# Performance work log

Hardware: AMD Instinct MI355X
Metric: run time of the kernel (lower is better)

Reference implementation:

```python
import jax, jax.numpy as jnp
import numpy as np

B, T = 512, 200          # batch (trials), time bins
N = 10000                # n_neurons
SI, DI = 100, 68         # static / dynamic input sizes
HS, HD = 256, 128        # hidden_dim_static / hidden_dim_dynamic
K = 1                    # output_size
D = 2 * HD + HS          # 512, routed-GEMM contraction dim


def setup_inputs() -> dict:
    key = jax.random.key(0)
    ks = jax.random.split(key, 19)
    g = lambda i, shape, s=0.05: (jax.random.normal(ks[i], shape, jnp.float32) * s)
    return dict(
        x_static=g(0, (B, SI), 1.0),
        x_dynamic=g(1, (B, T, DI), 1.0),
        neuron_order=jax.random.randint(ks[2], (B,), 0, N),
        w_s1=g(3, (HS, SI)), b_s1=g(4, (HS,)),
        w_s2=g(5, (HS, HS)), b_s2=g(6, (HS,)),
        w_dyn=g(7, (HD, DI)), b_dyn=g(8, (HD,)),
        w_ih_f=g(9, (HD, HD)), w_hh_f=g(10, (HD, HD)),
        b_ih_f=g(11, (HD,)), b_hh_f=g(12, (HD,)),
        w_ih_b=g(13, (HD, HD)), w_hh_b=g(14, (HD, HD)),
        b_ih_b=g(15, (HD,)), b_hh_b=g(16, (HD,)),
        neuron_weights=g(17, (N, D, K)),
        neuron_bias=g(18, (N, 1, K)),
    )


def _rnn_dir(x, w_ih, w_hh, b_ih, b_hh, reverse):
    # x: [B,T,H] -> outputs [B,T,H]; torch nn.RNN with nonlinearity='relu'
    xw = jnp.einsum('bth,oh->bto', x, w_ih) + b_ih + b_hh  # precompute input proj
    h0 = jnp.zeros((x.shape[0], w_hh.shape[0]), x.dtype)

    def step(h, xt):
        h = jax.nn.relu(xt + h @ w_hh.T)
        return h, h

    _, ys = jax.lax.scan(step, h0, jnp.swapaxes(xw, 0, 1), reverse=reverse)
    return jnp.swapaxes(ys, 0, 1)


def reference(x_static, x_dynamic, neuron_order,
              w_s1, b_s1, w_s2, b_s2, w_dyn, b_dyn,
              w_ih_f, w_hh_f, b_ih_f, b_hh_f,
              w_ih_b, w_hh_b, b_ih_b, b_hh_b,
              neuron_weights, neuron_bias):
    # static branch (dropout in eval mode -> identity)
    s = jax.nn.relu(x_static @ w_s1.T + b_s1)
    s = jax.nn.relu(s @ w_s2.T + b_s2)                      # [B,HS]
    # dynamic branch
    d = jax.nn.relu(jnp.einsum('bti,oi->bto', x_dynamic, w_dyn) + b_dyn)  # [B,T,HD]
    fwd = _rnn_dir(d, w_ih_f, w_hh_f, b_ih_f, b_hh_f, reverse=False)
    bwd = _rnn_dir(d, w_ih_b, w_hh_b, b_ih_b, b_hh_b, reverse=True)
    d = jax.nn.relu(jnp.concatenate([fwd, bwd], axis=-1))   # [B,T,2*HD]
    # tile static over time and concat
    s_t = jnp.broadcast_to(s[:, None, :], (s.shape[0], d.shape[1], s.shape[1]))
    final_input = jnp.concatenate([s_t, d], axis=-1)        # [B,T,D]
    # per-sample neuron weight gather + routed batched matmul + bias + ReLU
    Wn = neuron_weights[neuron_order]                       # [B,D,K]
    bn = neuron_bias[neuron_order]                          # [B,1,K]
    out = jnp.einsum('btd,bdk->btk', final_input, Wn) + bn  # [B,T,K]
    return jax.nn.relu(jnp.squeeze(out, -1))                # [B,T] (K=1)
```

## Files before the change

### kernel.cpp

```cpp
#include <hip/hip_runtime.h>
#include <cstdint>

constexpr int B = 512, T = 200, SI = 100, DI = 68, HS = 256, HD = 128, D = 512;
constexpr int BT = B * T;

typedef __attribute__((ext_vector_type(8))) short short8;
typedef __attribute__((ext_vector_type(4))) float floatx4;
typedef _Float16 half8 __attribute__((ext_vector_type(8)));
typedef _Float16 half2t __attribute__((ext_vector_type(2)));
typedef unsigned int uint2v __attribute__((ext_vector_type(2)));
typedef unsigned int uint4v __attribute__((ext_vector_type(4)));

#define DEV __device__ __forceinline__

DEV unsigned short f2bf(float f) {
    unsigned int x = __builtin_bit_cast(unsigned int, f);
    x += 0x7fffu + ((x >> 16) & 1u);
    return (unsigned short)(x >> 16);
}
DEV unsigned int pkbf(float a, float b) {
    return (unsigned int)f2bf(a) | ((unsigned int)f2bf(b) << 16);
}
DEV unsigned short f2h(float f) {
    return __builtin_bit_cast(unsigned short, (_Float16)f);
}
DEV half2t u2h2(unsigned int u) { return __builtin_bit_cast(half2t, u); }
DEV unsigned int pkh(float a, float b) {
    return __builtin_bit_cast(unsigned int, __builtin_amdgcn_cvt_pkrtz(a, b));
}
#if __has_builtin(__builtin_amdgcn_permlane32_swap) && __has_builtin(__builtin_amdgcn_permlane16_swap)
DEV void pl32swap(unsigned int& a, unsigned int& b) {
    uint2v r = __builtin_amdgcn_permlane32_swap(a, b, false, false);
    a = r[0]; b = r[1];
}
DEV void pl16swap(unsigned int& a, unsigned int& b) {
    uint2v r = __builtin_amdgcn_permlane16_swap(a, b, false, false);
    a = r[0]; b = r[1];
}
#else
DEV void pl32swap(unsigned int& a, unsigned int& b) {
    unsigned int na, nb;
    asm("v_mov_b32 %0, %2\n\t"
        "v_mov_b32 %1, %3\n\t"
        "v_permlane32_swap_b32 %0, %1"
        : "=&v"(na), "=&v"(nb) : "v"(a), "v"(b));
    a = na; b = nb;
}
DEV void pl16swap(unsigned int& a, unsigned int& b) {
    unsigned int na, nb;
    asm("v_mov_b32 %0, %2\n\t"
        "v_mov_b32 %1, %3\n\t"
        "v_permlane16_swap_b32 %0, %1"
        : "=&v"(na), "=&v"(nb) : "v"(a), "v"(b));
    a = na; b = nb;
}
#endif

__global__ __launch_bounds__(256) void k_prep(
    const float* __restrict__ wdyn,
    const float* __restrict__ wihf, const float* __restrict__ wihb,
    const float* __restrict__ whhf, const float* __restrict__ whhb,
    const float* __restrict__ bihf, const float* __restrict__ bhhf,
    const float* __restrict__ bihb, const float* __restrict__ bhhb,
    unsigned short* __restrict__ wdyn_bf, unsigned short* __restrict__ wih_bf,
    unsigned short* __restrict__ whh_h, float* __restrict__ bsum)
{
    int gid = blockIdx.x * 256 + threadIdx.x, gs = gridDim.x * 256;
    for (int i = gid; i < HD * 96; i += gs) {
        int r = i / 96, c = i - r * 96;
        wdyn_bf[i] = (c < DI) ? f2bf(wdyn[r * DI + c]) : 0;
    }
    for (int i = gid; i < 2 * HD * HD; i += gs) {
        const float* src = (i < HD * HD) ? wihf : wihb;
        wih_bf[i] = f2bf(src[i & (HD * HD - 1)]);
    }
    for (int i = gid; i < 2 * HD * HD; i += gs) {
        const float* src = (i < HD * HD) ? whhf : whhb;
        whh_h[i] = f2h(src[i & (HD * HD - 1)]);
    }
    for (int i = gid; i < 2 * HD; i += gs) {
        int z = i >> 7, n = i & (HD - 1);
        bsum[i] = z ? (bihb[n] + bhhb[n]) : (bihf[n] + bhhf[n]);
    }
}

__global__ __launch_bounds__(256) void k_static(
    const float* __restrict__ xs_g, const float* __restrict__ w1,
    const float* __restrict__ b1, const float* __restrict__ w2,
    const float* __restrict__ b2, const int* __restrict__ norder,
    const float* __restrict__ nw, const float* __restrict__ nb,
    float* __restrict__ statd)
{
    __shared__ __align__(16) float xs[SI];
    __shared__ __align__(16) float s1[HS];
    __shared__ __align__(16) float red[256];
    int b = blockIdx.x, t = threadIdx.x;
    if (t < SI) xs[t] = xs_g[b * SI + t];
    __syncthreads();
    float a = b1[t];
    const float4* w = (const float4*)(w1 + t * SI);
    const float4* xp4 = (const float4*)xs;
    #pragma unroll
    for (int i = 0; i < SI / 4; ++i) {
        float4 ww = w[i]; float4 xx = xp4[i];
        a += xx.x * ww.x + xx.y * ww.y + xx.z * ww.z + xx.w * ww.w;
    }
    s1[t] = fmaxf(a, 0.f);
    __syncthreads();
    float a2 = b2[t];
    const float4* w2p = (const float4*)(w2 + t * HS);
    const float4* s1p = (const float4*)s1;
    #pragma unroll 8
    for (int i = 0; i < HS / 4; ++i) {
        float4 ww = w2p[i]; float4 s = s1p[i];
        a2 += s.x * ww.x + s.y * ww.y + s.z * ww.z + s.w * ww.w;
    }
    float sv = fmaxf(a2, 0.f);
    int n = norder[b];
    red[t] = sv * nw[(size_t)n * D + t];
    __syncthreads();
    for (int s = 128; s > 0; s >>= 1) {
        if (t < s) red[t] += red[t + s];
        __syncthreads();
    }
    if (t == 0) statd[b] = red[0] + nb[n];
}

__global__ __launch_bounds__(256) void k_dxw(
    const float* __restrict__ xd,
    const unsigned short* __restrict__ wdyn_bf, const float* __restrict__ bdyn,
    const unsigned short* __restrict__ wih_bf, const float* __restrict__ bsum,
    unsigned short* __restrict__ xw)
{
    __shared__ __align__(16) unsigned short xb[64][104];
    __shared__ __align__(16) unsigned short dl[64][136];
    int tid = threadIdx.x;
    int R0 = blockIdx.x * 64;
    for (int i = tid; i < 64 * 104 / 8; i += 256)
        ((uint4v*)xb)[i] = uint4v{0u, 0u, 0u, 0u};
    __syncthreads();
    for (int i = tid; i < 64 * 17; i += 256) {
        int r = i / 17, c = i - r * 17;
        float4 v = *(const float4*)(xd + (size_t)(R0 + r) * DI + c * 4);
        uint2 pk;
        pk.x = pkbf(v.x, v.y);
        pk.y = pkbf(v.z, v.w);
        *(uint2*)&xb[r][c * 4] = pk;
    }
    __syncthreads();

    int lane = tid & 63, w = tid >> 6;
    int ln = lane & 15, q = lane >> 4;

    short8 xf[3];
    #pragma unroll
    for (int c = 0; c < 3; ++c)
        xf[c] = *(const short8*)&xb[w * 16 + ln][c * 32 + q * 8];
    #pragma unroll
    for (int j = 0; j < 8; ++j) {
        floatx4 a = {0.f, 0.f, 0.f, 0.f};
        #pragma unroll
        for (int c = 0; c < 3; ++c) {
            short8 wf = *(const short8*)(wdyn_bf + (size_t)(j * 16 + ln) * 96 + c * 32 + q * 8);
            a = __builtin_amdgcn_mfma_f32_16x16x32_bf16(wf, xf[c], a, 0, 0, 0);
        }
        float4 bd4 = *(const float4*)(bdyn + j * 16 + q * 4);
        uint2 pk;
        pk.x = pkbf(fmaxf(a[0] + bd4.x, 0.f), fmaxf(a[1] + bd4.y, 0.f));
        pk.y = pkbf(fmaxf(a[2] + bd4.z, 0.f), fmaxf(a[3] + bd4.w, 0.f));
        *(uint2*)&dl[w * 16 + ln][j * 16 + q * 4] = pk;
    }
    __syncthreads();

    short8 df[4];
    #pragma unroll
    for (int c = 0; c < 4; ++c)
        df[c] = *(const short8*)&dl[w * 16 + ln][c * 32 + q * 8];
    #pragma unroll
    for (int z = 0; z < 2; ++z) {
        const unsigned short* wih = wih_bf + (size_t)z * HD * HD;
        unsigned short* outp = xw + (size_t)z * BT * HD;
        int row = R0 + w * 16 + ln;
        #pragma unroll
        for (int j = 0; j < 8; ++j) {
            floatx4 a = {0.f, 0.f, 0.f, 0.f};
            #pragma unroll
            for (int c = 0; c < 4; ++c) {
                short8 wf = *(const short8*)(wih + (size_t)(j * 16 + ln) * HD + c * 32 + q * 8);
                a = __builtin_amdgcn_mfma_f32_16x16x32_bf16(wf, df[c], a, 0, 0, 0);
            }
            float4 b4 = *(const float4*)(bsum + z * HD + j * 16 + q * 4);
            uint2 hp;
            hp.x = (unsigned int)f2h(a[0] + b4.x) | ((unsigned int)f2h(a[1] + b4.y) << 16);
            hp.y = (unsigned int)f2h(a[2] + b4.z) | ((unsigned int)f2h(a[3] + b4.w) << 16);
            *(uint2*)(outp + (size_t)row * HD + j * 16 + q * 4) = hp;
        }
    }
}

__global__ __launch_bounds__(256, 1) void k_scan(
    const unsigned short* __restrict__ xw, const unsigned short* __restrict__ whh_h,
    const int* __restrict__ norder, const float* __restrict__ nw,
    float* __restrict__ accf, float* __restrict__ accb)
{
    __shared__ __align__(16) uint4v hxch[2][4][64];
    __shared__ __align__(16) float  pxch[2][4][16];

    int tid = threadIdx.x, w = tid >> 6, l = tid & 63, ln = l & 15, q = l >> 4;
    int dir = blockIdx.x >> 5, b0 = (blockIdx.x & 31) * 16;
    const unsigned short* whh = whh_h + (size_t)dir * HD * HD;
    float* acc = dir ? accb : accf;
    int segoff = dir ? (HS + HD) : HS;
    int j0 = 2 * w;

    half8 wfr[2][4];
    #pragma unroll
    for (int jj = 0; jj < 2; ++jj)
        #pragma unroll
        for (int c = 0; c < 4; ++c)
            wfr[jj][c] = *(const half8*)(whh + (size_t)((j0 + jj) * 16 + ln) * HD + c * 32 + q * 8);

    int nrow = norder[b0 + ln];
    float4 wnl[2];
    #pragma unroll
    for (int jj = 0; jj < 2; ++jj)
        wnl[jj] = *(const float4*)(nw + (size_t)nrow * D + segoff + (j0 + jj) * 16 + q * 4);

    half8 hf[4];
    uint4v zz = {0u, 0u, 0u, 0u};
    #pragma unroll
    for (int c = 0; c < 4; ++c) hf[c] = __builtin_bit_cast(half8, zz);

    const unsigned short* xp = xw + ((size_t)dir * BT + (size_t)(b0 + ln) * T) * HD;
    float* accp = acc + (size_t)(b0 + ln) * T;
    int tstart = dir ? (T - 1) : 0, dt = dir ? -1 : 1;

    uint2 xb0[2], xb1[2], xb2[2], xb3[2];
    auto ld = [&](uint2 (&xb)[2], int idx) {
        const unsigned short* pp = xp + (size_t)(tstart + dt * idx) * HD;
        #pragma unroll
        for (int jj = 0; jj < 2; ++jj)
            xb[jj] = *(const uint2*)(pp + (j0 + jj) * 16 + q * 4);
    };
    auto step = [&](uint2 (&xc)[2], int idx) {
        int t = tstart + dt * idx;
        int par = idx & 1;
        floatx4 a[2];
        #pragma unroll
        for (int jj = 0; jj < 2; ++jj) {
            half2t lo = u2h2(xc[jj].x), hi = u2h2(xc[jj].y);
            a[jj] = floatx4{(float)lo[0], (float)lo[1], (float)hi[0], (float)hi[1]};
        }
        #pragma unroll
        for (int cc = 0; cc < 4; ++cc)
            #pragma unroll
            for (int jj = 0; jj < 2; ++jj)
                a[jj] = __builtin_amdgcn_mfma_f32_16x16x32_f16(wfr[jj][cc], hf[cc], a[jj], 0, 0, 0);
        uint2 hp[2];
        float p = 0.f;
        #pragma unroll
        for (int jj = 0; jj < 2; ++jj) {
            float r0 = fmaxf(a[jj][0], 0.f), r1 = fmaxf(a[jj][1], 0.f);
            float r2 = fmaxf(a[jj][2], 0.f), r3 = fmaxf(a[jj][3], 0.f);
            hp[jj].x = pkh(r0, r1);
            hp[jj].y = pkh(r2, r3);
            float4 wn4 = wnl[jj];
            p += r0 * wn4.x + r1 * wn4.y + r2 * wn4.z + r3 * wn4.w;
        }
        unsigned int ax = hp[0].x, bx = hp[1].x;
        pl32swap(ax, bx); pl16swap(ax, bx);
        unsigned int ay = hp[0].y, by = hp[1].y;
        pl32swap(ay, by); pl16swap(ay, by);
        uint4v hw = {ax, ay, bx, by};
        hxch[par][w][l] = hw;
        unsigned int pa = __builtin_bit_cast(unsigned int, p), pb = pa;
        pl32swap(pa, pb);
        float ps = __builtin_bit_cast(float, pa) + __builtin_bit_cast(float, pb);
        unsigned int pc = __builtin_bit_cast(unsigned int, ps), pd = pc;
        pl16swap(pc, pd);
        float ptot = __builtin_bit_cast(float, pc) + __builtin_bit_cast(float, pd);
        if (l < 16) pxch[par][w][ln] = ptot;
        asm volatile("s_waitcnt lgkmcnt(0)" ::: "memory");
        __builtin_amdgcn_sched_barrier(0);
        __builtin_amdgcn_s_barrier();
        __builtin_amdgcn_sched_barrier(0);
        #pragma unroll
        for (int c = 0; c < 4; ++c)
            hf[c] = __builtin_bit_cast(half8, hxch[par][c][l]);
        if (w == 0) {
            float p2 = pxch[par][q][ln];
            unsigned int qa = __builtin_bit_cast(unsigned int, p2), qb = qa;
            pl32swap(qa, qb);
            float qs = __builtin_bit_cast(float, qa) + __builtin_bit_cast(float, qb);
            unsigned int qc = __builtin_bit_cast(unsigned int, qs), qd = qc;
            pl16swap(qc, qd);
            float qt = __builtin_bit_cast(float, qc) + __builtin_bit_cast(float, qd);
            if (l < 16) accp[t] = qt;
        }
    };

    ld(xb0, 0); ld(xb1, 1); ld(xb2, 2); ld(xb3, 3);
    for (int c = 0; c < T / 4 - 1; ++c) {
        int i0 = c * 4;
        step(xb0, i0);     ld(xb0, i0 + 4);
        step(xb1, i0 + 1); ld(xb1, i0 + 5);
        step(xb2, i0 + 2); ld(xb2, i0 + 6);
        step(xb3, i0 + 3); ld(xb3, i0 + 7);
    }
    step(xb0, T - 4);
    step(xb1, T - 3);
    step(xb2, T - 2);
    step(xb3, T - 1);
}

__global__ __launch_bounds__(256) void k_final(
    const float* __restrict__ statd, const float* __restrict__ accf,
    const float* __restrict__ accb, float* __restrict__ out)
{
    int idx = blockIdx.x * 256 + threadIdx.x;
    if (idx < BT) {
        int b = idx / T;
        out[idx] = fmaxf(statd[b] + accf[idx] + accb[idx], 0.f);
    }
}

extern "C" void kernel_launch(void* const* d_in, const int* in_sizes, int n_in,
                              void* d_out, int out_size, void* d_ws, size_t ws_size,
                              hipStream_t stream)
{
    const float* x_static  = (const float*)d_in[0];
    const float* x_dynamic = (const float*)d_in[1];
    const int*   norder    = (const int*)d_in[2];
    const float* w_s1   = (const float*)d_in[3];
    const float* b_s1   = (const float*)d_in[4];
    const float* w_s2   = (const float*)d_in[5];
    const float* b_s2   = (const float*)d_in[6];
    const float* w_dyn  = (const float*)d_in[7];
    const float* b_dyn  = (const float*)d_in[8];
    const float* w_ih_f = (const float*)d_in[9];
    const float* w_hh_f = (const float*)d_in[10];
    const float* b_ih_f = (const float*)d_in[11];
    const float* b_hh_f = (const float*)d_in[12];
    const float* w_ih_b = (const float*)d_in[13];
    const float* w_hh_b = (const float*)d_in[14];
    const float* b_ih_b = (const float*)d_in[15];
    const float* b_hh_b = (const float*)d_in[16];
    const float* nw     = (const float*)d_in[17];
    const float* nb     = (const float*)d_in[18];
    float* out = (float*)d_out;

    char* ws = (char*)d_ws;
    float* statd = (float*)ws;
    float* accf  = (float*)(ws + 2048);
    float* accb  = (float*)(ws + 2048 + (size_t)BT * 4);
    unsigned short* xw = (unsigned short*)(ws + 2048 + (size_t)BT * 8);
    size_t xw_bytes = (size_t)2 * BT * HD * 2;
    unsigned short* wdyn_bf = (unsigned short*)(ws + 2048 + (size_t)BT * 8 + xw_bytes);
    unsigned short* wih_bf  = wdyn_bf + HD * 96;
    unsigned short* whh_h   = wih_bf + 2 * HD * HD;
    float* bsum = (float*)(whh_h + 2 * HD * HD);

    hipLaunchKernelGGL(k_prep, dim3(64), dim3(256), 0, stream,
                       w_dyn, w_ih_f, w_ih_b, w_hh_f, w_hh_b,
                       b_ih_f, b_hh_f, b_ih_b, b_hh_b,
                       wdyn_bf, wih_bf, whh_h, bsum);
    hipLaunchKernelGGL(k_static, dim3(B), dim3(256), 0, stream,
                       x_static, w_s1, b_s1, w_s2, b_s2, norder, nw, nb, statd);
    hipLaunchKernelGGL(k_dxw, dim3(BT / 64), dim3(256), 0, stream,
                       x_dynamic, wdyn_bf, b_dyn, wih_bf, bsum, xw);
    hipLaunchKernelGGL(k_scan, dim3(64), dim3(256), 0, stream,
                       xw, whh_h, norder, nw, accf, accb);
    hipLaunchKernelGGL(k_final, dim3((BT + 255) / 256), dim3(256), 0, stream,
                       statd, accf, accb, out);
}
```

Measured before the change: 299.2 us.

## Interleave forward and backward RNN scans in one block, drop partial-sum LDS exchange

```diff
diff --git a/kernel.cpp b/kernel.cpp
--- a/kernel.cpp
+++ b/kernel.cpp
@@ -203,114 +203,143 @@
     const int* __restrict__ norder, const float* __restrict__ nw,
     float* __restrict__ accf, float* __restrict__ accb)
 {
-    __shared__ __align__(16) uint4v hxch[2][4][64];
-    __shared__ __align__(16) float  pxch[2][4][16];
+    __shared__ __align__(16) uint4v hxch[2][2][4][64];
 
     int tid = threadIdx.x, w = tid >> 6, l = tid & 63, ln = l & 15, q = l >> 4;
-    int dir = blockIdx.x >> 5, b0 = (blockIdx.x & 31) * 16;
-    const unsigned short* whh = whh_h + (size_t)dir * HD * HD;
-    float* acc = dir ? accb : accf;
-    int segoff = dir ? (HS + HD) : HS;
+    int b0 = blockIdx.x * 16;
     int j0 = 2 * w;
 
-    half8 wfr[2][4];
-    #pragma unroll
-    for (int jj = 0; jj < 2; ++jj)
-        #pragma unroll
-        for (int c = 0; c < 4; ++c)
-            wfr[jj][c] = *(const half8*)(whh + (size_t)((j0 + jj) * 16 + ln) * HD + c * 32 + q * 8);
+    half8 wfr[2][2][4];
+    #pragma unroll
+    for (int d = 0; d < 2; ++d)
+        #pragma unroll
+        for (int jj = 0; jj < 2; ++jj)
+            #pragma unroll
+            for (int c = 0; c < 4; ++c)
+                wfr[d][jj][c] = *(const half8*)(whh_h + (size_t)d * HD * HD +
+                    (size_t)((j0 + jj) * 16 + ln) * HD + c * 32 + q * 8);
 
     int nrow = norder[b0 + ln];
-    float4 wnl[2];
-    #pragma unroll
-    for (int jj = 0; jj < 2; ++jj)
-        wnl[jj] = *(const float4*)(nw + (size_t)nrow * D + segoff + (j0 + jj) * 16 + q * 4);
-
-    half8 hf[4];
+    float4 wnl[2][2];
+    #pragma unroll
+    for (int d = 0; d < 2; ++d)
+        #pragma unroll
+        for (int jj = 0; jj < 2; ++jj)
+            wnl[d][jj] = *(const float4*)(nw + (size_t)nrow * D + (d ? HS + HD : HS) +
+                                          (j0 + jj) * 16 + q * 4);
+
+    half8 hfF[4], hfB[4];
     uint4v zz = {0u, 0u, 0u, 0u};
     #pragma unroll
-    for (int c = 0; c < 4; ++c) hf[c] = __builtin_bit_cast(half8, zz);
-
-    const unsigned short* xp = xw + ((size_t)dir * BT + (size_t)(b0 + ln) * T) * HD;
-    float* accp = acc + (size_t)(b0 + ln) * T;
-    int tstart = dir ? (T - 1) : 0, dt = dir ? -1 : 1;
-
-    uint2 xb0[2], xb1[2], xb2[2], xb3[2];
-    auto ld = [&](uint2 (&xb)[2], int idx) {
-        const unsigned short* pp = xp + (size_t)(tstart + dt * idx) * HD;
-        #pragma unroll
-        for (int jj = 0; jj < 2; ++jj)
-            xb[jj] = *(const uint2*)(pp + (j0 + jj) * 16 + q * 4);
+    for (int c = 0; c < 4; ++c) {
+        hfF[c] = __builtin_bit_cast(half8, zz);
+        hfB[c] = __builtin_bit_cast(half8, zz);
+    }
+
+    const unsigned short* xpF = xw + ((size_t)(b0 + ln) * T) * HD;
+    const unsigned short* xpB = xw + ((size_t)BT + (size_t)(b0 + ln) * T) * HD;
+    float* accpF = accf + (size_t)w * BT + (size_t)(b0 + ln) * T;
+    float* accpB = accb + (size_t)w * BT + (size_t)(b0 + ln) * T;
+
+    uint2 xF0[2], xF1[2], xF2[2], xF3[2];
+    uint2 xB0[2], xB1[2], xB2[2], xB3[2];
+    auto ld = [&](uint2 (&xF)[2], uint2 (&xB)[2], int idx) {
+        const unsigned short* ppF = xpF + (size_t)idx * HD;
+        const unsigned short* ppB = xpB + (size_t)(T - 1 - idx) * HD;
+        #pragma unroll
+        for (int jj = 0; jj < 2; ++jj) {
+            xF[jj] = *(const uint2*)(ppF + (j0 + jj) * 16 + q * 4);
+            xB[jj] = *(const uint2*)(ppB + (j0 + jj) * 16 + q * 4);
+        }
     };
-    auto step = [&](uint2 (&xc)[2], int idx) {
-        int t = tstart + dt * idx;
+    auto step = [&](uint2 (&xF)[2], uint2 (&xB)[2], int idx) {
+        int tF = idx, tB = T - 1 - idx;
         int par = idx & 1;
-        floatx4 a[2];
+        floatx4 aF[2], aB[2];
         #pragma unroll
         for (int jj = 0; jj < 2; ++jj) {
-            half2t lo = u2h2(xc[jj].x), hi = u2h2(xc[jj].y);
-            a[jj] = floatx4{(float)lo[0], (float)lo[1], (float)hi[0], (float)hi[1]};
-        }
-        #pragma unroll
-        for (int cc = 0; cc < 4; ++cc)
+            half2t lo = u2h2(xF[jj].x), hi = u2h2(xF[jj].y);
+            aF[jj] = floatx4{(float)lo[0], (float)lo[1], (float)hi[0], (float)hi[1]};
+            half2t lo2 = u2h2(xB[jj].x), hi2 = u2h2(xB[jj].y);
+            aB[jj] = floatx4{(float)lo2[0], (float)lo2[1], (float)hi2[0], (float)hi2[1]};
+        }
+        #pragma unroll
+        for (int cc = 0; cc < 4; ++cc) {
             #pragma unroll
             for (int jj = 0; jj < 2; ++jj)
-                a[jj] = __builtin_amdgcn_mfma_f32_16x16x32_f16(wfr[jj][cc], hf[cc], a[jj], 0, 0, 0);
-        uint2 hp[2];
-        float p = 0.f;
+                aF[jj] = __builtin_amdgcn_mfma_f32_16x16x32_f16(wfr[0][jj][cc], hfF[cc], aF[jj], 0, 0, 0);
+            #pragma unroll
+            for (int jj = 0; jj < 2; ++jj)
+                aB[jj] = __builtin_amdgcn_mfma_f32_16x16x32_f16(wfr[1][jj][cc], hfB[cc], aB[jj], 0, 0, 0);
+        }
+        uint2 hpF[2], hpB[2];
+        float pF = 0.f, pB = 0.f;
         #pragma unroll
         for (int jj = 0; jj < 2; ++jj) {
-            float r0 = fmaxf(a[jj][0], 0.f), r1 = fmaxf(a[jj][1], 0.f);
-            float r2 = fmaxf(a[jj][2], 0.f), r3 = fmaxf(a[jj][3], 0.f);
-            hp[jj].x = pkh(r0, r1);
-            hp[jj].y = pkh(r2, r3);
-            float4 wn4 = wnl[jj];
-            p += r0 * wn4.x + r1 * wn4.y + r2 * wn4.z + r3 * wn4.w;
-        }
-        unsigned int ax = hp[0].x, bx = hp[1].x;
-        pl32swap(ax, bx); pl16swap(ax, bx);
-        unsigned int ay = hp[0].y, by = hp[1].y;
-        pl32swap(ay, by); pl16swap(ay, by);
-        uint4v hw = {ax, ay, bx, by};
-        hxch[par][w][l] = hw;
-        unsigned int pa = __builtin_bit_cast(unsigned int, p), pb = pa;
+            float r0 = fmaxf(aF[jj][0], 0.f), r1 = fmaxf(aF[jj][1], 0.f);
+            float r2 = fmaxf(aF[jj][2], 0.f), r3 = fmaxf(aF[jj][3], 0.f);
+            hpF[jj].x = pkh(r0, r1); hpF[jj].y = pkh(r2, r3);
+            float4 wn4 = wnl[0][jj];
+            pF += r0 * wn4.x + r1 * wn4.y + r2 * wn4.z + r3 * wn4.w;
+            float s0 = fmaxf(aB[jj][0], 0.f), s1 = fmaxf(aB[jj][1], 0.f);
+            float s2 = fmaxf(aB[jj][2], 0.f), s3 = fmaxf(aB[jj][3], 0.f);
+            hpB[jj].x = pkh(s0, s1); hpB[jj].y = pkh(s2, s3);
+            float4 wm4 = wnl[1][jj];
+            pB += s0 * wm4.x + s1 * wm4.y + s2 * wm4.z + s3 * wm4.w;
+        }
+        {
+            unsigned int ax = hpF[0].x, bx = hpF[1].x;
+            pl32swap(ax, bx); pl16swap(ax, bx);
+            unsigned int ay = hpF[0].y, by = hpF[1].y;
+            pl32swap(ay, by); pl16swap(ay, by);
+            hxch[par][0][w][l] = uint4v{ax, ay, bx, by};
+        }
+        {
+            unsigned int ax = hpB[0].x, bx = hpB[1].x;
+            pl32swap(ax, bx); pl16swap(ax, bx);
+            unsigned int ay = hpB[0].y, by = hpB[1].y;
+            pl32swap(ay, by); pl16swap(ay, by);
+            hxch[par][1][w][l] = uint4v{ax, ay, bx, by};
+        }
+        unsigned int pa = __builtin_bit_cast(unsigned int, pF), pb = pa;
         pl32swap(pa, pb);
         float ps = __builtin_bit_cast(float, pa) + __builtin_bit_cast(float, pb);
         unsigned int pc = __builtin_bit_cast(unsigned int, ps), pd = pc;
         pl16swap(pc, pd);
-        float ptot = __builtin_bit_cast(float, pc) + __builtin_bit_cast(float, pd);
-        if (l < 16) pxch[par][w][ln] = ptot;
+        float ptF = __builtin_bit_cast(float, pc) + __builtin_bit_cast(float, pd);
+        unsigned int qa = __builtin_bit_cast(unsigned int, pB), qb = qa;
+        pl32swap(qa, qb);
+        float qs = __builtin_bit_cast(float, qa) + __builtin_bit_cast(float, qb);
+        unsigned int qc = __builtin_bit_cast(unsigned int, qs), qd = qc;
+        pl16swap(qc, qd);
+        float ptB = __builtin_bit_cast(float, qc) + __builtin_bit_cast(float, qd);
+        if (l < 16) {
+            accpF[tF] = ptF;
+            accpB[tB] = ptB;
+        }
         asm volatile("s_waitcnt lgkmcnt(0)" ::: "memory");
         __builtin_amdgcn_sched_barrier(0);
         __builtin_amdgcn_s_barrier();
         __builtin_amdgcn_sched_barrier(0);
         #pragma unroll
-        for (int c = 0; c < 4; ++c)
-            hf[c] = __builtin_bit_cast(half8, hxch[par][c][l]);
-        if (w == 0) {
-            float p2 = pxch[par][q][ln];
-            unsigned int qa = __builtin_bit_cast(unsigned int, p2), qb = qa;
-            pl32swap(qa, qb);
-            float qs = __builtin_bit_cast(float, qa) + __builtin_bit_cast(float, qb);
-            unsigned int qc = __builtin_bit_cast(unsigned int, qs), qd = qc;
-            pl16swap(qc, qd);
-            float qt = __builtin_bit_cast(float, qc) + __builtin_bit_cast(float, qd);
-            if (l < 16) accp[t] = qt;
+        for (int c = 0; c < 4; ++c) {
+            hfF[c] = __builtin_bit_cast(half8, hxch[par][0][c][l]);
+            hfB[c] = __builtin_bit_cast(half8, hxch[par][1][c][l]);
         }
     };
 
-    ld(xb0, 0); ld(xb1, 1); ld(xb2, 2); ld(xb3, 3);
+    ld(xF0, xB0, 0); ld(xF1, xB1, 1); ld(xF2, xB2, 2); ld(xF3, xB3, 3);
     for (int c = 0; c < T / 4 - 1; ++c) {
         int i0 = c * 4;
-        step(xb0, i0);     ld(xb0, i0 + 4);
-        step(xb1, i0 + 1); ld(xb1, i0 + 5);
-        step(xb2, i0 + 2); ld(xb2, i0 + 6);
-        step(xb3, i0 + 3); ld(xb3, i0 + 7);
-    }
-    step(xb0, T - 4);
-    step(xb1, T - 3);
-    step(xb2, T - 2);
-    step(xb3, T - 1);
+        step(xF0, xB0, i0);     ld(xF0, xB0, i0 + 4);
+        step(xF1, xB1, i0 + 1); ld(xF1, xB1, i0 + 5);
+        step(xF2, xB2, i0 + 2); ld(xF2, xB2, i0 + 6);
+        step(xF3, xB3, i0 + 3); ld(xF3, xB3, i0 + 7);
+    }
+    step(xF0, xB0, T - 4);
+    step(xF1, xB1, T - 3);
+    step(xF2, xB2, T - 2);
+    step(xF3, xB3, T - 1);
 }
 
 __global__ __launch_bounds__(256) void k_final(
@@ -320,7 +349,11 @@
     int idx = blockIdx.x * 256 + threadIdx.x;
     if (idx < BT) {
         int b = idx / T;
-        out[idx] = fmaxf(statd[b] + accf[idx] + accb[idx], 0.f);
+        float s = statd[b];
+        #pragma unroll
+        for (int w = 0; w < 4; ++w)
+            s += accf[(size_t)w * BT + idx] + accb[(size_t)w * BT + idx];
+        out[idx] = fmaxf(s, 0.f);
     }
 }
 
@@ -352,10 +385,10 @@
     char* ws = (char*)d_ws;
     float* statd = (float*)ws;
     float* accf  = (float*)(ws + 2048);
-    float* accb  = (float*)(ws + 2048 + (size_t)BT * 4);
-    unsigned short* xw = (unsigned short*)(ws + 2048 + (size_t)BT * 8);
+    float* accb  = (float*)(ws + 2048 + (size_t)4 * BT * 4);
+    unsigned short* xw = (unsigned short*)(ws + 2048 + (size_t)8 * BT * 4);
     size_t xw_bytes = (size_t)2 * BT * HD * 2;
-    unsigned short* wdyn_bf = (unsigned short*)(ws + 2048 + (size_t)BT * 8 + xw_bytes);
+    unsigned short* wdyn_bf = (unsigned short*)(ws + 2048 + (size_t)8 * BT * 4 + xw_bytes);
     unsigned short* wih_bf  = wdyn_bf + HD * 96;
     unsigned short* whh_h   = wih_bf + 2 * HD * HD;
     float* bsum = (float*)(whh_h + 2 * HD * HD);
@@ -368,7 +401,7 @@
                        x_static, w_s1, b_s1, w_s2, b_s2, norder, nw, nb, statd);
     hipLaunchKernelGGL(k_dxw, dim3(BT / 64), dim3(256), 0, stream,
                        x_dynamic, wdyn_bf, b_dyn, wih_bf, bsum, xw);
-    hipLaunchKernelGGL(k_scan, dim3(64), dim3(256), 0, stream,
+    hipLaunchKernelGGL(k_scan, dim3(32), dim3(256), 0, stream,
                        xw, whh_h, norder, nw, accf, accb);
     hipLaunchKernelGGL(k_final, dim3((BT + 255) / 256), dim3(256), 0, stream,
                        statd, accf, accb, out);
```

Result: slower. 348.5 us (+16.5%).

## Split RNN scan across 8 waves per block and defer projection reduction

Applied to the files above, without the earlier changes.

```diff
diff --git a/kernel.cpp b/kernel.cpp
--- a/kernel.cpp
+++ b/kernel.cpp
@@ -198,88 +198,70 @@
     }
 }
 
-__global__ __launch_bounds__(256, 1) void k_scan(
+__global__ __launch_bounds__(512, 1) void k_scan(
     const unsigned short* __restrict__ xw, const unsigned short* __restrict__ whh_h,
     const int* __restrict__ norder, const float* __restrict__ nw,
     float* __restrict__ accf, float* __restrict__ accb)
 {
     __shared__ __align__(16) uint4v hxch[2][4][64];
-    __shared__ __align__(16) float  pxch[2][4][16];
 
     int tid = threadIdx.x, w = tid >> 6, l = tid & 63, ln = l & 15, q = l >> 4;
     int dir = blockIdx.x >> 5, b0 = (blockIdx.x & 31) * 16;
     const unsigned short* whh = whh_h + (size_t)dir * HD * HD;
-    float* acc = dir ? accb : accf;
+    float* acc = (dir ? accb : accf) + (size_t)w * BT;
     int segoff = dir ? (HS + HD) : HS;
-    int j0 = 2 * w;
-
-    half8 wfr[2][4];
-    #pragma unroll
-    for (int jj = 0; jj < 2; ++jj)
-        #pragma unroll
-        for (int c = 0; c < 4; ++c)
-            wfr[jj][c] = *(const half8*)(whh + (size_t)((j0 + jj) * 16 + ln) * HD + c * 32 + q * 8);
+
+    half8 wfr[4];
+    #pragma unroll
+    for (int c = 0; c < 4; ++c)
+        wfr[c] = *(const half8*)(whh + (size_t)(w * 16 + ln) * HD + c * 32 + q * 8);
 
     int nrow = norder[b0 + ln];
-    float4 wnl[2];
-    #pragma unroll
-    for (int jj = 0; jj < 2; ++jj)
-        wnl[jj] = *(const float4*)(nw + (size_t)nrow * D + segoff + (j0 + jj) * 16 + q * 4);
+    float4 wnl = *(const float4*)(nw + (size_t)nrow * D + segoff + w * 16 + q * 4);
 
     half8 hf[4];
     uint4v zz = {0u, 0u, 0u, 0u};
     #pragma unroll
     for (int c = 0; c < 4; ++c) hf[c] = __builtin_bit_cast(half8, zz);
 
-    const unsigned short* xp = xw + ((size_t)dir * BT + (size_t)(b0 + ln) * T) * HD;
+    const unsigned short* xp = xw + ((size_t)dir * BT + (size_t)(b0 + ln) * T) * HD
+                               + w * 16 + q * 4;
     float* accp = acc + (size_t)(b0 + ln) * T;
     int tstart = dir ? (T - 1) : 0, dt = dir ? -1 : 1;
 
-    uint2 xb0[2], xb1[2], xb2[2], xb3[2];
-    auto ld = [&](uint2 (&xb)[2], int idx) {
-        const unsigned short* pp = xp + (size_t)(tstart + dt * idx) * HD;
-        #pragma unroll
-        for (int jj = 0; jj < 2; ++jj)
-            xb[jj] = *(const uint2*)(pp + (j0 + jj) * 16 + q * 4);
+    int wc = w >> 1;
+    int qp = 2 * (w & 1) + (q >> 1);
+    int boff = (q & 1) * 8;
+
+    uint2 x0, x1, x2, x3;
+    auto ld = [&](uint2& xb, int idx) {
+        xb = *(const uint2*)(xp + (size_t)(tstart + dt * idx) * HD);
     };
-    auto step = [&](uint2 (&xc)[2], int idx) {
+    auto step = [&](uint2& xc, int idx) {
         int t = tstart + dt * idx;
         int par = idx & 1;
-        floatx4 a[2];
-        #pragma unroll
-        for (int jj = 0; jj < 2; ++jj) {
-            half2t lo = u2h2(xc[jj].x), hi = u2h2(xc[jj].y);
-            a[jj] = floatx4{(float)lo[0], (float)lo[1], (float)hi[0], (float)hi[1]};
-        }
-        #pragma unroll
-        for (int cc = 0; cc < 4; ++cc)
-            #pragma unroll
-            for (int jj = 0; jj < 2; ++jj)
-                a[jj] = __builtin_amdgcn_mfma_f32_16x16x32_f16(wfr[jj][cc], hf[cc], a[jj], 0, 0, 0);
-        uint2 hp[2];
-        float p = 0.f;
-        #pragma unroll
-        for (int jj = 0; jj < 2; ++jj) {
-            float r0 = fmaxf(a[jj][0], 0.f), r1 = fmaxf(a[jj][1], 0.f);
-            float r2 = fmaxf(a[jj][2], 0.f), r3 = fmaxf(a[jj][3], 0.f);
-            hp[jj].x = pkh(r0, r1);
-            hp[jj].y = pkh(r2, r3);
-            float4 wn4 = wnl[jj];
-            p += r0 * wn4.x + r1 * wn4.y + r2 * wn4.z + r3 * wn4.w;
-        }
-        unsigned int ax = hp[0].x, bx = hp[1].x;
-        pl32swap(ax, bx); pl16swap(ax, bx);
-        unsigned int ay = hp[0].y, by = hp[1].y;
-        pl32swap(ay, by); pl16swap(ay, by);
-        uint4v hw = {ax, ay, bx, by};
-        hxch[par][w][l] = hw;
+        half2t lo = u2h2(xc.x), hi = u2h2(xc.y);
+        floatx4 a0 = {(float)lo[0], (float)lo[1], (float)hi[0], (float)hi[1]};
+        floatx4 a1 = {0.f, 0.f, 0.f, 0.f};
+        a0 = __builtin_amdgcn_mfma_f32_16x16x32_f16(wfr[0], hf[0], a0, 0, 0, 0);
+        a1 = __builtin_amdgcn_mfma_f32_16x16x32_f16(wfr[1], hf[1], a1, 0, 0, 0);
+        a0 = __builtin_amdgcn_mfma_f32_16x16x32_f16(wfr[2], hf[2], a0, 0, 0, 0);
+        a1 = __builtin_amdgcn_mfma_f32_16x16x32_f16(wfr[3], hf[3], a1, 0, 0, 0);
+        floatx4 a = a0 + a1;
+        float r0 = fmaxf(a[0], 0.f), r1 = fmaxf(a[1], 0.f);
+        float r2 = fmaxf(a[2], 0.f), r3 = fmaxf(a[3], 0.f);
+        uint2 hp;
+        hp.x = pkh(r0, r1);
+        hp.y = pkh(r2, r3);
+        *(uint2*)((char*)&hxch[par][wc][qp * 16 + ln] + boff) = hp;
+        float p = r0 * wnl.x + r1 * wnl.y + r2 * wnl.z + r3 * wnl.w;
         unsigned int pa = __builtin_bit_cast(unsigned int, p), pb = pa;
         pl32swap(pa, pb);
         float ps = __builtin_bit_cast(float, pa) + __builtin_bit_cast(float, pb);
         unsigned int pc = __builtin_bit_cast(unsigned int, ps), pd = pc;
         pl16swap(pc, pd);
         float ptot = __builtin_bit_cast(float, pc) + __builtin_bit_cast(float, pd);
-        if (l < 16) pxch[par][w][ln] = ptot;
+        if (l < 16) accp[t] = ptot;
         asm volatile("s_waitcnt lgkmcnt(0)" ::: "memory");
         __builtin_amdgcn_sched_barrier(0);
         __builtin_amdgcn_s_barrier();
@@ -287,30 +269,20 @@
         #pragma unroll
         for (int c = 0; c < 4; ++c)
             hf[c] = __builtin_bit_cast(half8, hxch[par][c][l]);
-        if (w == 0) {
-            float p2 = pxch[par][q][ln];
-            unsigned int qa = __builtin_bit_cast(unsigned int, p2), qb = qa;
-            pl32swap(qa, qb);
-            float qs = __builtin_bit_cast(float, qa) + __builtin_bit_cast(float, qb);
-            unsigned int qc = __builtin_bit_cast(unsigned int, qs), qd = qc;
-            pl16swap(qc, qd);
-            float qt = __builtin_bit_cast(float, qc) + __builtin_bit_cast(float, qd);
-            if (l < 16) accp[t] = qt;
-        }
     };
 
-    ld(xb0, 0); ld(xb1, 1); ld(xb2, 2); ld(xb3, 3);
+    ld(x0, 0); ld(x1, 1); ld(x2, 2); ld(x3, 3);
     for (int c = 0; c < T / 4 - 1; ++c) {
         int i0 = c * 4;
-        step(xb0, i0);     ld(xb0, i0 + 4);
-        step(xb1, i0 + 1); ld(xb1, i0 + 5);
-        step(xb2, i0 + 2); ld(xb2, i0 + 6);
-        step(xb3, i0 + 3); ld(xb3, i0 + 7);
-    }
-    step(xb0, T - 4);
-    step(xb1, T - 3);
-    step(xb2, T - 2);
-    step(xb3, T - 1);
+        step(x0, i0);     ld(x0, i0 + 4);
+        step(x1, i0 + 1); ld(x1, i0 + 5);
+        step(x2, i0 + 2); ld(x2, i0 + 6);
+        step(x3, i0 + 3); ld(x3, i0 + 7);
+    }
+    step(x0, T - 4);
+    step(x1, T - 3);
+    step(x2, T - 2);
+    step(x3, T - 1);
 }
 
 __global__ __launch_bounds__(256) void k_final(
@@ -320,7 +292,11 @@
     int idx = blockIdx.x * 256 + threadIdx.x;
     if (idx < BT) {
         int b = idx / T;
-        out[idx] = fmaxf(statd[b] + accf[idx] + accb[idx], 0.f);
+        float s = statd[b];
+        #pragma unroll
+        for (int w = 0; w < 8; ++w)
+            s += accf[(size_t)w * BT + idx] + accb[(size_t)w * BT + idx];
+        out[idx] = fmaxf(s, 0.f);
     }
 }
 
@@ -352,10 +328,10 @@
     char* ws = (char*)d_ws;
     float* statd = (float*)ws;
     float* accf  = (float*)(ws + 2048);
-    float* accb  = (float*)(ws + 2048 + (size_t)BT * 4);
-    unsigned short* xw = (unsigned short*)(ws + 2048 + (size_t)BT * 8);
+    float* accb  = (float*)(ws + 2048 + (size_t)8 * BT * 4);
+    unsigned short* xw = (unsigned short*)(ws + 2048 + (size_t)16 * BT * 4);
     size_t xw_bytes = (size_t)2 * BT * HD * 2;
-    unsigned short* wdyn_bf = (unsigned short*)(ws + 2048 + (size_t)BT * 8 + xw_bytes);
+    unsigned short* wdyn_bf = (unsigned short*)(ws + 2048 + (size_t)16 * BT * 4 + xw_bytes);
     unsigned short* wih_bf  = wdyn_bf + HD * 96;
     unsigned short* whh_h   = wih_bf + 2 * HD * HD;
     float* bsum = (float*)(whh_h + 2 * HD * HD);
@@ -368,7 +344,7 @@
                        x_static, w_s1, b_s1, w_s2, b_s2, norder, nw, nb, statd);
     hipLaunchKernelGGL(k_dxw, dim3(BT / 64), dim3(256), 0, stream,
                        x_dynamic, wdyn_bf, b_dyn, wih_bf, bsum, xw);
-    hipLaunchKernelGGL(k_scan, dim3(64), dim3(256), 0, stream,
+    hipLaunchKernelGGL(k_scan, dim3(64), dim3(512), 0, stream,
                        xw, whh_h, norder, nw, accf, accb);
     hipLaunchKernelGGL(k_final, dim3((BT + 255) / 256), dim3(256), 0, stream,
                        statd, accf, accb, out);
```

New measurement: 278.2 us. 7.0% less time.

## Fuse projection, static branch and RNN scan into producer-consumer persistent kernel

Applied to the files above, without the earlier changes.

```diff
diff --git a/kernel.cpp b/kernel.cpp
--- a/kernel.cpp
+++ b/kernel.cpp
@@ -3,6 +3,8 @@
 
 constexpr int B = 512, T = 200, SI = 100, DI = 68, HS = 256, HD = 128, D = 512;
 constexpr int BT = B * T;
+constexpr int NTILE = BT / 64;
+constexpr int NCONS = 64, NPROD = 192;
 
 typedef __attribute__((ext_vector_type(8))) short short8;
 typedef __attribute__((ext_vector_type(4))) float floatx4;
@@ -63,7 +65,8 @@
     const float* __restrict__ bihf, const float* __restrict__ bhhf,
     const float* __restrict__ bihb, const float* __restrict__ bhhb,
     unsigned short* __restrict__ wdyn_bf, unsigned short* __restrict__ wih_bf,
-    unsigned short* __restrict__ whh_h, float* __restrict__ bsum)
+    unsigned short* __restrict__ whh_h, float* __restrict__ bsum,
+    int* __restrict__ flags)
 {
     int gid = blockIdx.x * 256 + threadIdx.x, gs = gridDim.x * 256;
     for (int i = gid; i < HD * 96; i += gs) {
@@ -82,136 +85,154 @@
         int z = i >> 7, n = i & (HD - 1);
         bsum[i] = z ? (bihb[n] + bhhb[n]) : (bihf[n] + bhhf[n]);
     }
-}
-
-__global__ __launch_bounds__(256) void k_static(
-    const float* __restrict__ xs_g, const float* __restrict__ w1,
-    const float* __restrict__ b1, const float* __restrict__ w2,
-    const float* __restrict__ b2, const int* __restrict__ norder,
-    const float* __restrict__ nw, const float* __restrict__ nb,
-    float* __restrict__ statd)
-{
-    __shared__ __align__(16) float xs[SI];
-    __shared__ __align__(16) float s1[HS];
-    __shared__ __align__(16) float red[256];
-    int b = blockIdx.x, t = threadIdx.x;
-    if (t < SI) xs[t] = xs_g[b * SI + t];
-    __syncthreads();
-    float a = b1[t];
-    const float4* w = (const float4*)(w1 + t * SI);
-    const float4* xp4 = (const float4*)xs;
-    #pragma unroll
-    for (int i = 0; i < SI / 4; ++i) {
-        float4 ww = w[i]; float4 xx = xp4[i];
-        a += xx.x * ww.x + xx.y * ww.y + xx.z * ww.z + xx.w * ww.w;
-    }
-    s1[t] = fmaxf(a, 0.f);
-    __syncthreads();
-    float a2 = b2[t];
-    const float4* w2p = (const float4*)(w2 + t * HS);
-    const float4* s1p = (const float4*)s1;
-    #pragma unroll 8
-    for (int i = 0; i < HS / 4; ++i) {
-        float4 ww = w2p[i]; float4 s = s1p[i];
-        a2 += s.x * ww.x + s.y * ww.y + s.z * ww.z + s.w * ww.w;
-    }
-    float sv = fmaxf(a2, 0.f);
-    int n = norder[b];
-    red[t] = sv * nw[(size_t)n * D + t];
-    __syncthreads();
-    for (int s = 128; s > 0; s >>= 1) {
-        if (t < s) red[t] += red[t + s];
-        __syncthreads();
-    }
-    if (t == 0) statd[b] = red[0] + nb[n];
-}
-
-__global__ __launch_bounds__(256) void k_dxw(
+    for (int i = gid; i < 256; i += gs) flags[i] = 0;
+}
+
+__global__ __launch_bounds__(256, 1) void k_fused(
     const float* __restrict__ xd,
     const unsigned short* __restrict__ wdyn_bf, const float* __restrict__ bdyn,
     const unsigned short* __restrict__ wih_bf, const float* __restrict__ bsum,
-    unsigned short* __restrict__ xw)
+    unsigned short* __restrict__ xw, const unsigned short* __restrict__ whh_h,
+    const int* __restrict__ norder, const float* __restrict__ nw,
+    float* __restrict__ accf, float* __restrict__ accb,
+    int* __restrict__ flags,
+    const float* __restrict__ xs_g, const float* __restrict__ w1,
+    const float* __restrict__ b1, const float* __restrict__ w2,
+    const float* __restrict__ b2, const float* __restrict__ nb,
+    float* __restrict__ statd)
 {
     __shared__ __align__(16) unsigned short xb[64][104];
     __shared__ __align__(16) unsigned short dl[64][136];
+    __shared__ __align__(16) uint4v hxch[2][4][64];
+
     int tid = threadIdx.x;
-    int R0 = blockIdx.x * 64;
-    for (int i = tid; i < 64 * 104 / 8; i += 256)
-        ((uint4v*)xb)[i] = uint4v{0u, 0u, 0u, 0u};
-    __syncthreads();
-    for (int i = tid; i < 64 * 17; i += 256) {
-        int r = i / 17, c = i - r * 17;
-        float4 v = *(const float4*)(xd + (size_t)(R0 + r) * DI + c * 4);
-        uint2 pk;
-        pk.x = pkbf(v.x, v.y);
-        pk.y = pkbf(v.z, v.w);
-        *(uint2*)&xb[r][c * 4] = pk;
-    }
-    __syncthreads();
-
-    int lane = tid & 63, w = tid >> 6;
-    int ln = lane & 15, q = lane >> 4;
-
-    short8 xf[3];
-    #pragma unroll
-    for (int c = 0; c < 3; ++c)
-        xf[c] = *(const short8*)&xb[w * 16 + ln][c * 32 + q * 8];
-    #pragma unroll
-    for (int j = 0; j < 8; ++j) {
-        floatx4 a = {0.f, 0.f, 0.f, 0.f};
-        #pragma unroll
-        for (int c = 0; c < 3; ++c) {
-            short8 wf = *(const short8*)(wdyn_bf + (size_t)(j * 16 + ln) * 96 + c * 32 + q * 8);
-            a = __builtin_amdgcn_mfma_f32_16x16x32_bf16(wf, xf[c], a, 0, 0, 0);
+    int lane = tid & 63, wv = tid >> 6, ln = lane & 15, q = lane >> 4;
+
+    if (blockIdx.x >= NCONS) {
+        int p = blockIdx.x - NCONS;
+        short8 wdf[8][3];
+        #pragma unroll
+        for (int j = 0; j < 8; ++j)
+            #pragma unroll
+            for (int c = 0; c < 3; ++c)
+                wdf[j][c] = *(const short8*)(wdyn_bf + (size_t)(j * 16 + ln) * 96 + c * 32 + q * 8);
+        short8 wif[2][8][4];
+        #pragma unroll
+        for (int z = 0; z < 2; ++z)
+            #pragma unroll
+            for (int j = 0; j < 8; ++j)
+                #pragma unroll
+                for (int c = 0; c < 4; ++c)
+                    wif[z][j][c] = *(const short8*)(wih_bf + (size_t)z * HD * HD +
+                        (size_t)(j * 16 + ln) * HD + c * 32 + q * 8);
+        for (int i = tid; i < 64 * 104 / 8; i += 256)
+            ((uint4v*)xb)[i] = uint4v{0u, 0u, 0u, 0u};
+
+        for (int m = p; m < NTILE; m += NPROD) {
+            int slab = m >> 3, sub = m & 7;
+            int t = (slab & 1) ? (T - 1 - (slab >> 1)) : (slab >> 1);
+            int b0 = sub * 64;
+            __syncthreads();
+            for (int i = tid; i < 64 * 17; i += 256) {
+                int r = i / 17, c2 = i - r * 17;
+                float4 v = *(const float4*)(xd + ((size_t)(b0 + r) * T + t) * DI + c2 * 4);
+                uint2 pk;
+                pk.x = pkbf(v.x, v.y);
+                pk.y = pkbf(v.z, v.w);
+                *(uint2*)&xb[r][c2 * 4] = pk;
+            }
+            __syncthreads();
+            short8 xf[3];
+            #pragma unroll
+            for (int c = 0; c < 3; ++c)
+                xf[c] = *(const short8*)&xb[wv * 16 + ln][c * 32 + q * 8];
+            #pragma unroll
+            for (int j = 0; j < 8; ++j) {
+                floatx4 a = {0.f, 0.f, 0.f, 0.f};
+                #pragma unroll
+                for (int c = 0; c < 3; ++c)
+                    a = __builtin_amdgcn_mfma_f32_16x16x32_bf16(wdf[j][c], xf[c], a, 0, 0, 0);
+                float4 bd4 = *(const float4*)(bdyn + j * 16 + q * 4);
+                uint2 pk;
+                pk.x = pkbf(fmaxf(a[0] + bd4.x, 0.f), fmaxf(a[1] + bd4.y, 0.f));
+                pk.y = pkbf(fmaxf(a[2] + bd4.z, 0.f), fmaxf(a[3] + bd4.w, 0.f));
+                *(uint2*)&dl[wv * 16 + ln][j * 16 + q * 4] = pk;
+            }
+            __syncthreads();
+            short8 df[4];
+            #pragma unroll
+            for (int c = 0; c < 4; ++c)
+                df[c] = *(const short8*)&dl[wv * 16 + ln][c * 32 + q * 8];
+            int brow = b0 + wv * 16 + ln;
+            #pragma unroll
+            for (int z = 0; z < 2; ++z) {
+                unsigned short* outp = xw + (size_t)z * BT * HD;
+                #pragma unroll
+                for (int j = 0; j < 8; ++j) {
+                    floatx4 a = {0.f, 0.f, 0.f, 0.f};
+                    #pragma unroll
+                    for (int c = 0; c < 4; ++c)
+                        a = __builtin_amdgcn_mfma_f32_16x16x32_bf16(wif[z][j][c], df[c], a, 0, 0, 0);
+                    float4 b4 = *(const float4*)(bsum + z * HD + j * 16 + q * 4);
+                    uint2 hp;
+                    hp.x = (unsigned int)f2h(a[0] + b4.x) | ((unsigned int)f2h(a[1] + b4.y) << 16);
+                    hp.y = (unsigned int)f2h(a[2] + b4.z) | ((unsigned int)f2h(a[3] + b4.w) << 16);
+                    *(uint2*)(outp + ((size_t)brow * T + t) * HD + j * 16 + q * 4) = hp;
+                }
+            }
+            __syncthreads();
+            if (tid == 0)
+                __hip_atomic_fetch_add(&flags[t], 1, __ATOMIC_RELEASE,
+                                       __HIP_MEMORY_SCOPE_AGENT);
         }
-        float4 bd4 = *(const float4*)(bdyn + j * 16 + q * 4);
-        uint2 pk;
-        pk.x = pkbf(fmaxf(a[0] + bd4.x, 0.f), fmaxf(a[1] + bd4.y, 0.f));
-        pk.y = pkbf(fmaxf(a[2] + bd4.z, 0.f), fmaxf(a[3] + bd4.w, 0.f));
-        *(uint2*)&dl[w * 16 + ln][j * 16 + q * 4] = pk;
-    }
-    __syncthreads();
-
-    short8 df[4];
-    #pragma unroll
-    for (int c = 0; c < 4; ++c)
-        df[c] = *(const short8*)&dl[w * 16 + ln][c * 32 + q * 8];
-    #pragma unroll
-    for (int z = 0; z < 2; ++z) {
-        const unsigned short* wih = wih_bf + (size_t)z * HD * HD;
-        unsigned short* outp = xw + (size_t)z * BT * HD;
-        int row = R0 + w * 16 + ln;
-        #pragma unroll
-        for (int j = 0; j < 8; ++j) {
-            floatx4 a = {0.f, 0.f, 0.f, 0.f};
-            #pragma unroll
-            for (int c = 0; c < 4; ++c) {
-                short8 wf = *(const short8*)(wih + (size_t)(j * 16 + ln) * HD + c * 32 + q * 8);
-                a = __builtin_amdgcn_mfma_f32_16x16x32_bf16(wf, df[c], a, 0, 0, 0);
-            }
-            float4 b4 = *(const float4*)(bsum + z * HD + j * 16 + q * 4);
-            uint2 hp;
-            hp.x = (unsigned int)f2h(a[0] + b4.x) | ((unsigned int)f2h(a[1] + b4.y) << 16);
-            hp.y = (unsigned int)f2h(a[2] + b4.z) | ((unsigned int)f2h(a[3] + b4.w) << 16);
-            *(uint2*)(outp + (size_t)row * HD + j * 16 + q * 4) = hp;
+        return;
+    }
+
+    int g = blockIdx.x;
+    int dirv = g >> 5, b0 = (g & 31) * 16;
+
+    {
+        float* sxs = (float*)hxch;
+        float* ss1 = sxs + 104;
+        float* sred = ss1 + 256;
+        for (int bb = g * 8; bb < g * 8 + 8; ++bb) {
+            if (tid < SI) sxs[tid] = xs_g[bb * SI + tid];
+            __syncthreads();
+            float a = b1[tid];
+            const float4* wr = (const float4*)(w1 + tid * SI);
+            const float4* xp4 = (const float4*)sxs;
+            #pragma unroll
+            for (int i = 0; i < SI / 4; ++i) {
+                float4 ww = wr[i]; float4 xx = xp4[i];
+                a += xx.x * ww.x + xx.y * ww.y + xx.z * ww.z + xx.w * ww.w;
+            }
+            ss1[tid] = fmaxf(a, 0.f);
+            __syncthreads();
+            float a2 = b2[tid];
+            const float4* w2p = (const float4*)(w2 + tid * HS);
+            const float4* s1p = (const float4*)ss1;
+            #pragma unroll 8
+            for (int i = 0; i < HS / 4; ++i) {
+                float4 ww = w2p[i]; float4 s = s1p[i];
+                a2 += s.x * ww.x + s.y * ww.y + s.z * ww.z + s.w * ww.w;
+            }
+            float sv = fmaxf(a2, 0.f);
+            int n = norder[bb];
+            sred[tid] = sv * nw[(size_t)n * D + tid];
+            __syncthreads();
+            for (int s = 128; s > 0; s >>= 1) {
+                if (tid < s) sred[tid] += sred[tid + s];
+                __syncthreads();
+            }
+            if (tid == 0) statd[bb] = sred[0] + nb[n];
+            __syncthreads();
         }
     }
-}
-
-__global__ __launch_bounds__(256, 1) void k_scan(
-    const unsigned short* __restrict__ xw, const unsigned short* __restrict__ whh_h,
-    const int* __restrict__ norder, const float* __restrict__ nw,
-    float* __restrict__ accf, float* __restrict__ accb)
-{
-    __shared__ __align__(16) uint4v hxch[2][4][64];
-    __shared__ __align__(16) float  pxch[2][4][16];
-
-    int tid = threadIdx.x, w = tid >> 6, l = tid & 63, ln = l & 15, q = l >> 4;
-    int dir = blockIdx.x >> 5, b0 = (blockIdx.x & 31) * 16;
-    const unsigned short* whh = whh_h + (size_t)dir * HD * HD;
-    float* acc = dir ? accb : accf;
-    int segoff = dir ? (HS + HD) : HS;
-    int j0 = 2 * w;
+
+    const unsigned short* whh = whh_h + (size_t)dirv * HD * HD;
+    float* accp = (dirv ? accb : accf) + (size_t)wv * BT + (size_t)(b0 + ln) * T;
+    int segoff = dirv ? (HS + HD) : HS;
+    int j0 = 2 * wv;
 
     half8 wfr[2][4];
     #pragma unroll
@@ -231,16 +252,34 @@
     #pragma unroll
     for (int c = 0; c < 4; ++c) hf[c] = __builtin_bit_cast(half8, zz);
 
-    const unsigned short* xp = xw + ((size_t)dir * BT + (size_t)(b0 + ln) * T) * HD;
-    float* accp = acc + (size_t)(b0 + ln) * T;
-    int tstart = dir ? (T - 1) : 0, dt = dir ? -1 : 1;
-
-    uint2 xb0[2], xb1[2], xb2[2], xb3[2];
-    auto ld = [&](uint2 (&xb)[2], int idx) {
+    const unsigned short* xp = xw + ((size_t)dirv * BT + (size_t)(b0 + ln) * T) * HD;
+    int tstart = dirv ? (T - 1) : 0, dt = dirv ? -1 : 1;
+
+    auto gate = [&](int idx) {
+        if (tid == 0) {
+            #pragma unroll 1
+            for (int k = 0; k < 4; ++k) {
+                int ii = idx + k;
+                if (ii >= T) break;
+                int t = tstart + dt * ii;
+                for (int it = 0; it < (1 << 20); ++it) {
+                    if (__hip_atomic_load(&flags[t], __ATOMIC_ACQUIRE,
+                                          __HIP_MEMORY_SCOPE_AGENT) >= 8) break;
+                    __builtin_amdgcn_s_sleep(8);
+                }
+            }
+        }
+        __builtin_amdgcn_sched_barrier(0);
+        __builtin_amdgcn_s_barrier();
+        __builtin_amdgcn_sched_barrier(0);
+    };
+
+    uint2 x0[2], x1[2], x2[2], x3[2];
+    auto ld = [&](uint2 (&xc)[2], int idx) {
         const unsigned short* pp = xp + (size_t)(tstart + dt * idx) * HD;
         #pragma unroll
         for (int jj = 0; jj < 2; ++jj)
-            xb[jj] = *(const uint2*)(pp + (j0 + jj) * 16 + q * 4);
+            xc[jj] = *(const uint2*)(pp + (j0 + jj) * 16 + q * 4);
     };
     auto step = [&](uint2 (&xc)[2], int idx) {
         int t = tstart + dt * idx;
@@ -257,7 +296,7 @@
             for (int jj = 0; jj < 2; ++jj)
                 a[jj] = __builtin_amdgcn_mfma_f32_16x16x32_f16(wfr[jj][cc], hf[cc], a[jj], 0, 0, 0);
         uint2 hp[2];
-        float p = 0.f;
+        float pdot = 0.f;
         #pragma unroll
         for (int jj = 0; jj < 2; ++jj) {
             float r0 = fmaxf(a[jj][0], 0.f), r1 = fmaxf(a[jj][1], 0.f);
@@ -265,52 +304,43 @@
             hp[jj].x = pkh(r0, r1);
             hp[jj].y = pkh(r2, r3);
             float4 wn4 = wnl[jj];
-            p += r0 * wn4.x + r1 * wn4.y + r2 * wn4.z + r3 * wn4.w;
+            pdot += r0 * wn4.x + r1 * wn4.y + r2 * wn4.z + r3 * wn4.w;
         }
         unsigned int ax = hp[0].x, bx = hp[1].x;
         pl32swap(ax, bx); pl16swap(ax, bx);
         unsigned int ay = hp[0].y, by = hp[1].y;
         pl32swap(ay, by); pl16swap(ay, by);
-        uint4v hw = {ax, ay, bx, by};
-        hxch[par][w][l] = hw;
-        unsigned int pa = __builtin_bit_cast(unsigned int, p), pb = pa;
+        hxch[par][wv][lane] = uint4v{ax, ay, bx, by};
+        unsigned int pa = __builtin_bit_cast(unsigned int, pdot), pb = pa;
         pl32swap(pa, pb);
         float ps = __builtin_bit_cast(float, pa) + __builtin_bit_cast(float, pb);
         unsigned int pc = __builtin_bit_cast(unsigned int, ps), pd = pc;
         pl16swap(pc, pd);
         float ptot = __builtin_bit_cast(float, pc) + __builtin_bit_cast(float, pd);
-        if (l < 16) pxch[par][w][ln] = ptot;
+        if (lane < 16) accp[t] = ptot;
         asm volatile("s_waitcnt lgkmcnt(0)" ::: "memory");
         __builtin_amdgcn_sched_barrier(0);
         __builtin_amdgcn_s_barrier();
         __builtin_amdgcn_sched_barrier(0);
         #pragma unroll
         for (int c = 0; c < 4; ++c)
-            hf[c] = __builtin_bit_cast(half8, hxch[par][c][l]);
-        if (w == 0) {
-            float p2 = pxch[par][q][ln];
-            unsigned int qa = __builtin_bit_cast(unsigned int, p2), qb = qa;
-            pl32swap(qa, qb);
-            float qs = __builtin_bit_cast(float, qa) + __builtin_bit_cast(float, qb);
-            unsigned int qc = __builtin_bit_cast(unsigned int, qs), qd = qc;
-            pl16swap(qc, qd);
-            float qt = __builtin_bit_cast(float, qc) + __builtin_bit_cast(float, qd);
-            if (l < 16) accp[t] = qt;
-        }
+            hf[c] = __builtin_bit_cast(half8, hxch[par][c][lane]);
     };
 
-    ld(xb0, 0); ld(xb1, 1); ld(xb2, 2); ld(xb3, 3);
+    gate(0);
+    ld(x0, 0); ld(x1, 1); ld(x2, 2); ld(x3, 3);
     for (int c = 0; c < T / 4 - 1; ++c) {
         int i0 = c * 4;
-        step(xb0, i0);     ld(xb0, i0 + 4);
-        step(xb1, i0 + 1); ld(xb1, i0 + 5);
-        step(xb2, i0 + 2); ld(xb2, i0 + 6);
-        step(xb3, i0 + 3); ld(xb3, i0 + 7);
-    }
-    step(xb0, T - 4);
-    step(xb1, T - 3);
-    step(xb2, T - 2);
-    step(xb3, T - 1);
+        gate(i0 + 4);
+        step(x0, i0);     ld(x0, i0 + 4);
+        step(x1, i0 + 1); ld(x1, i0 + 5);
+        step(x2, i0 + 2); ld(x2, i0 + 6);
+        step(x3, i0 + 3); ld(x3, i0 + 7);
+    }
+    step(x0, T - 4);
+    step(x1, T - 3);
+    step(x2, T - 2);
+    step(x3, T - 1);
 }
 
 __global__ __launch_bounds__(256) void k_final(
@@ -320,7 +350,11 @@
     int idx = blockIdx.x * 256 + threadIdx.x;
     if (idx < BT) {
         int b = idx / T;
-        out[idx] = fmaxf(statd[b] + accf[idx] + accb[idx], 0.f);
+        float s = statd[b];
+        #pragma unroll
+        for (int w = 0; w < 4; ++w)
+            s += accf[(size_t)w * BT + idx] + accb[(size_t)w * BT + idx];
+        out[idx] = fmaxf(s, 0.f);
     }
 }
 
@@ -352,24 +386,23 @@
     char* ws = (char*)d_ws;
     float* statd = (float*)ws;
     float* accf  = (float*)(ws + 2048);
-    float* accb  = (float*)(ws + 2048 + (size_t)BT * 4);
-    unsigned short* xw = (unsigned short*)(ws + 2048 + (size_t)BT * 8);
+    float* accb  = (float*)(ws + 2048 + (size_t)4 * BT * 4);
+    unsigned short* xw = (unsigned short*)(ws + 2048 + (size_t)8 * BT * 4);
     size_t xw_bytes = (size_t)2 * BT * HD * 2;
-    unsigned short* wdyn_bf = (unsigned short*)(ws + 2048 + (size_t)BT * 8 + xw_bytes);
+    unsigned short* wdyn_bf = (unsigned short*)(ws + 2048 + (size_t)8 * BT * 4 + xw_bytes);
     unsigned short* wih_bf  = wdyn_bf + HD * 96;
     unsigned short* whh_h   = wih_bf + 2 * HD * HD;
-    float* bsum = (float*)(whh_h + 2 * HD * HD);
+    float* bsum  = (float*)(whh_h + 2 * HD * HD);
+    int*   flags = (int*)(bsum + 2 * HD);
 
     hipLaunchKernelGGL(k_prep, dim3(64), dim3(256), 0, stream,
                        w_dyn, w_ih_f, w_ih_b, w_hh_f, w_hh_b,
                        b_ih_f, b_hh_f, b_ih_b, b_hh_b,
-                       wdyn_bf, wih_bf, whh_h, bsum);
-    hipLaunchKernelGGL(k_static, dim3(B), dim3(256), 0, stream,
-                       x_static, w_s1, b_s1, w_s2, b_s2, norder, nw, nb, statd);
-    hipLaunchKernelGGL(k_dxw, dim3(BT / 64), dim3(256), 0, stream,
-                       x_dynamic, wdyn_bf, b_dyn, wih_bf, bsum, xw);
-    hipLaunchKernelGGL(k_scan, dim3(64), dim3(256), 0, stream,
-                       xw, whh_h, norder, nw, accf, accb);
+                       wdyn_bf, wih_bf, whh_h, bsum, flags);
+    hipLaunchKernelGGL(k_fused, dim3(256), dim3(256), 0, stream,
+                       x_dynamic, wdyn_bf, b_dyn, wih_bf, bsum,
+                       xw, whh_h, norder, nw, accf, accb, flags,
+                       x_static, w_s1, b_s1, w_s2, b_s2, nb, statd);
     hipLaunchKernelGGL(k_final, dim3((BT + 255) / 256), dim3(256), 0, stream,
                        statd, accf, accb, out);
 }
```

After: 370.0 us. 23.7% more time.
